# Kernel optimization log

Hardware: AMD Instinct MI355X
Metric: run time of the kernel (lower is better)

The kernel has to match this reference:

```python
import jax, jax.numpy as jnp
import numpy as np

N_NODES = 512   # nodes per graph == feature dim (GCNConv in_channels)
B = 64          # batch of graphs
HID = 16        # action_hidden_dim == edge_hidden_dim
E = 262144      # total edges (~8 per node)
N_TOTAL = B * N_NODES


def _gcn(x, W, b, src, dst, n):
    """PyG GCNConv: add self loops, sym-normalize, x@W -> scatter-add, +bias."""
    h = x @ W  # [n, hid]
    loop = jnp.arange(n)
    s = jnp.concatenate([src, loop])
    d = jnp.concatenate([dst, loop])
    deg = jax.ops.segment_sum(jnp.ones((s.shape[0],), x.dtype), d, num_segments=n)
    dinv = jnp.where(deg > 0, jax.lax.rsqrt(deg), 0.0)
    norm = dinv[s] * dinv[d]
    out = jax.ops.segment_sum(norm[:, None] * h[s], d, num_segments=n)
    return out + b


def _group_sum(t, ptr):
    # cumsum-based segment sum over contiguous node blocks, as in the original
    c = jnp.concatenate([jnp.zeros((1,) + t.shape[1:], t.dtype), jnp.cumsum(t, axis=0)], axis=0)
    return c[ptr[1:]] - c[ptr[:-1]]


def setup_inputs() -> dict:
    key = jax.random.key(0)
    k = jax.random.split(key, 4)
    node_feature = jax.random.normal(k[0], (N_TOTAL, N_NODES), jnp.float32)
    edge_index = jax.random.randint(k[1], (E, 2), 0, N_TOTAL)  # global node ids
    node_index = jnp.arange(N_TOTAL)                            # sorted global ids
    batch_ptr = jnp.arange(B + 1) * N_NODES
    scale = np.float32(1.0 / np.sqrt(N_NODES))
    W_act = jax.random.normal(k[2], (N_NODES, HID), jnp.float32) * scale
    b_act = jnp.zeros((HID,), jnp.float32)
    W_edge = jax.random.normal(k[3], (N_NODES, HID), jnp.float32) * scale
    b_edge = jnp.zeros((HID,), jnp.float32)
    return {"node_feature": node_feature, "W_act": W_act, "b_act": b_act,
            "W_edge": W_edge, "b_edge": b_edge, "edge_index": edge_index,
            "node_index": node_index, "batch_ptr": batch_ptr}


def reference(node_feature, W_act, b_act, W_edge, b_edge, edge_index, node_index, batch_ptr):
    n_total, n_nodes = node_feature.shape
    n_graphs = batch_ptr.shape[0] - 1
    # remap global ids -> local positions; node_index sorted => searchsorted
    # is exactly the original's torch.where(edge_index[...,None]==node_index)[2]
    ei = jnp.searchsorted(node_index, edge_index)  # [E, 2]
    src, dst = ei[:, 0], ei[:, 1]
    # action-type head: GCN -> mean over hidden -> per-graph segment sum
    at = _gcn(node_feature, W_act, b_act, src, dst, n_total)          # [N, hid]
    at = _group_sum(jnp.mean(at, axis=-1, keepdims=True), batch_ptr)  # [B, 1]
    # edge head: GCN -> per-graph pairwise inner products
    eh = _gcn(node_feature, W_edge, b_edge, src, dst, n_total)
    eh = eh.reshape(n_graphs, n_nodes, -1)                            # [B, n, hid]
    pair = jnp.einsum('bnf,bmf->bnm', eh, eh)                         # [B, n, n]
    edge_actions = pair.reshape(n_graphs, n_nodes * n_nodes)
    return jnp.concatenate([at, edge_actions], axis=-1)               # [B, 1 + n*n]
```

## Files before the change

### kernel.cpp

```cpp
#include <hip/hip_runtime.h>
#include <hip/hip_bf16.h>
#include <stdint.h>

#define NTOT   32768
#define NNODE  512
#define NGRAPH 64
#define HID    16
#define NEDGE  262144
#define OROW   262145
#define CAP    32
#define GEMM_BLOCKS 1024

typedef __attribute__((ext_vector_type(4)))  float f32x4;
typedef __attribute__((ext_vector_type(16))) float f32x16;
typedef __attribute__((ext_vector_type(8)))  short bf16x8;

union U8 { bf16x8 v; unsigned int u[4]; };

static __device__ __forceinline__ unsigned int pkbf(float lo, float hi) {
  union { __hip_bfloat162 h; unsigned int u; } c;
  c.h = __float22bfloat162_rn(float2{lo, hi});
  return c.u;
}
static __device__ __forceinline__ unsigned short f2bf(float f) {
  union { float f; unsigned int u; } v; v.f = f;
  unsigned int u = v.u;
  u += 0x7fffu + ((u >> 16) & 1u);
  return (unsigned short)(u >> 16);
}

__global__ __launch_bounds__(512) void k_gemmfill(const float* __restrict__ x,
                                                  const float* __restrict__ Wa,
                                                  const float* __restrict__ We,
                                                  const int* __restrict__ ei,
                                                  int* __restrict__ cnt,
                                                  int* __restrict__ csr,
                                                  float* __restrict__ h_act,
                                                  float* __restrict__ h_edge) {
  __shared__ float red[64 * 129];
  if (blockIdx.x >= GEMM_BLOCKS) {
    int i = (blockIdx.x - GEMM_BLOCKS) * 512 + threadIdx.x;
    int4 e2 = ((const int4*)ei)[i];
    int p0 = atomicAdd(&cnt[e2.y], 1);
    if (p0 < CAP) csr[e2.y * CAP + p0] = e2.x;
    int p1 = atomicAdd(&cnt[e2.w], 1);
    if (p1 < CAP) csr[e2.w * CAP + p1] = e2.z;
    return;
  }
  int row0 = blockIdx.x * 32;
  int w = threadIdx.x >> 6, lane = threadIdx.x & 63;
  int r = lane & 31, g = lane >> 5;
  const float* xp = x + (size_t)(row0 + r) * 512 + w * 64 + g * 8;
  const float* Wp = ((r < 16) ? Wa : We) + (r & 15);
  int k0 = w * 64 + g * 8;
  f32x16 acc = {0,0,0,0,0,0,0,0,0,0,0,0,0,0,0,0};
  #pragma unroll
  for (int kb = 0; kb < 4; ++kb) {
    f32x4 x0 = *(const f32x4*)(xp + kb * 16);
    f32x4 x1 = *(const f32x4*)(xp + kb * 16 + 4);
    U8 a, b;
    a.u[0] = pkbf(x0[0], x0[1]);
    a.u[1] = pkbf(x0[2], x0[3]);
    a.u[2] = pkbf(x1[0], x1[1]);
    a.u[3] = pkbf(x1[2], x1[3]);
    int kk = k0 + kb * 16;
    #pragma unroll
    for (int p = 0; p < 4; ++p)
      b.u[p] = pkbf(Wp[(kk + 2 * p) * 16], Wp[(kk + 2 * p + 1) * 16]);
    acc = __builtin_amdgcn_mfma_f32_32x32x16_bf16(a.v, b.v, acc, 0, 0, 0);
  }
  #pragma unroll
  for (int i = 0; i < 16; ++i) red[lane * 129 + w * 16 + i] = acc[i];
  __syncthreads();
  int rl = threadIdx.x & 63, q = threadIdx.x >> 6;
  float s0 = 0.f, s1 = 0.f;
  #pragma unroll
  for (int ww = 0; ww < 8; ++ww) {
    s0 += red[rl * 129 + ww * 16 + q * 2];
    s1 += red[rl * 129 + ww * 16 + q * 2 + 1];
  }
  int col = rl & 31, gg = rl >> 5;
  float* hp = (col < 16) ? h_act : h_edge;
  int c = col & 15;
  int i0 = q * 2, i1 = i0 + 1;
  hp[(row0 + (i0 & 3) + 8 * (i0 >> 2) + 4 * gg) * HID + c] = s0;
  hp[(row0 + (i1 & 3) + 8 * (i1 >> 2) + 4 * gg) * HID + c] = s1;
}

__global__ __launch_bounds__(256) void k_gather(const int* __restrict__ cnt,
                                                const int* __restrict__ csr,
                                                const float* __restrict__ h_act,
                                                const float* __restrict__ h_edge,
                                                const float* __restrict__ ba,
                                                const float* __restrict__ be,
                                                unsigned short* __restrict__ ebf,
                                                float* __restrict__ at_graph) {
  int tid = blockIdx.x * 256 + threadIdx.x;
  int node = tid >> 4, f = tid & 15;
  int deg = cnt[node];
  float dd = rsqrtf(1.0f + (float)deg);
  int nd = min(deg, CAP);
  float w0 = dd * dd;
  float acc_a = w0 * h_act[(size_t)node * HID + f];
  float acc_e = w0 * h_edge[(size_t)node * HID + f];
  const int* bucket = csr + (size_t)node * CAP;
  for (int k = 0; k < nd; ++k) {
    int s = bucket[k];
    float w = rsqrtf(1.0f + (float)cnt[s]) * dd;
    acc_a += w * h_act[(size_t)s * HID + f];
    acc_e += w * h_edge[(size_t)s * HID + f];
  }
  float va = acc_a + ba[f];
  float ve = acc_e + be[f];
  ebf[tid] = f2bf(ve);
  #pragma unroll
  for (int m = 1; m < 16; m <<= 1) va += __shfl_xor(va, m, 64);
  __shared__ float ablk[16];
  if (f == 0) ablk[threadIdx.x >> 4] = va;
  __syncthreads();
  if (threadIdx.x == 0) {
    float s = 0.f;
    #pragma unroll
    for (int i = 0; i < 16; ++i) s += ablk[i];
    unsafeAtomicAdd(&at_graph[blockIdx.x >> 5], s);
  }
}

__global__ __launch_bounds__(256) void k_gram(const unsigned short* __restrict__ ebf,
                                              const float* __restrict__ at_graph,
                                              float* __restrict__ out) {
  int b = blockIdx.x;
  int graph = b >> 3, sub = b & 7;
  if (sub == 0 && threadIdx.x == 0)
    out[(size_t)graph * OROW] = at_graph[graph] * (1.0f / 16.0f);
  int wave = threadIdx.x >> 6, lane = threadIdx.x & 63;
  int r = lane & 15, g = lane >> 4;
  int n0 = (sub * 4 + wave) * 16;
  const unsigned short* eb = ebf + graph * NNODE * HID;
  size_t obase = (size_t)graph * OROW + 1;
  bf16x8 zf = {0,0,0,0,0,0,0,0};
  bf16x8 a = zf;
  if (g < 2) a = *(const bf16x8*)(eb + (n0 + r) * HID + g * 8);
  for (int mt = 0; mt < 32; ++mt) {
    int m0 = mt * 16;
    bf16x8 bb = zf;
    if (g < 2) bb = *(const bf16x8*)(eb + (m0 + r) * HID + g * 8);
    f32x4 acc = {0, 0, 0, 0};
    acc = __builtin_amdgcn_mfma_f32_16x16x32_bf16(a, bb, acc, 0, 0, 0);
    #pragma unroll
    for (int j = 0; j < 4; ++j) {
      int n = n0 + g * 4 + j;
      out[obase + (size_t)n * NNODE + m0 + r] = acc[j];
    }
  }
}

extern "C" void kernel_launch(void* const* d_in, const int* in_sizes, int n_in,
                              void* d_out, int out_size, void* d_ws, size_t ws_size,
                              hipStream_t stream) {
  const float* x  = (const float*)d_in[0];
  const float* Wa = (const float*)d_in[1];
  const float* ba = (const float*)d_in[2];
  const float* We = (const float*)d_in[3];
  const float* be = (const float*)d_in[4];
  const int* ei   = (const int*)d_in[5];
  float* out = (float*)d_out;

  char* w = (char*)d_ws;
  float* h_act    = (float*)(w);
  float* h_edge   = (float*)(w + (2u << 20));
  unsigned short* ebf = (unsigned short*)(w + (4u << 20));
  int*   csr      = (int*)  (w + (5u << 20));
  int*   cnt      = (int*)  (w + (9u << 20));
  float* at_graph = (float*)(w + (9u << 20) + (128u << 10));

  hipMemsetAsync(cnt, 0, 32768 * 4 + 64 * 4, stream);
  k_gemmfill<<<1280, 512, 0, stream>>>(x, Wa, We, ei, cnt, csr, h_act, h_edge);
  k_gather  <<<2048, 256, 0, stream>>>(cnt, csr, h_act, h_edge, ba, be, ebf, at_graph);
  k_gram    <<<512, 256, 0, stream>>>(ebf, at_graph, out);
}
```

Before: 72.13 us.

## Collapse action head to per-node hidden mean, vectorize CSR loads, split gram blocks

Because the action head only needs the mean over hidden features, the GEMM kernel now reduces the action projection to one scalar per node. The gather kernel then aggregates that scalar instead of a 16-wide vector, and the bias sum is folded into the final per-graph output. The gather loop reads neighbor indices as int4 with masked tails. The gram kernel doubles its grid by splitting columns into halves. The aim is to cut gather memory traffic and raise parallelism in the output-write stage, at the cost of one extra memset and changed float summation order.

```diff
diff --git a/kernel.cpp b/kernel.cpp
--- a/kernel.cpp
+++ b/kernel.cpp
@@ -35,8 +35,8 @@
                                                   const int* __restrict__ ei,
                                                   int* __restrict__ cnt,
                                                   int* __restrict__ csr,
-                                                  float* __restrict__ h_act,
-                                                  float* __restrict__ h_edge) {
+                                                  float* __restrict__ h_edge,
+                                                  float* __restrict__ hm) {
   __shared__ float red[64 * 129];
   if (blockIdx.x >= GEMM_BLOCKS) {
     int i = (blockIdx.x - GEMM_BLOCKS) * 512 + threadIdx.x;
@@ -79,19 +79,30 @@
     s0 += red[rl * 129 + ww * 16 + q * 2];
     s1 += red[rl * 129 + ww * 16 + q * 2 + 1];
   }
+  float t0 = s0, t1 = s1;
+  #pragma unroll
+  for (int m = 1; m < 16; m <<= 1) {
+    t0 += __shfl_xor(t0, m, 64);
+    t1 += __shfl_xor(t1, m, 64);
+  }
   int col = rl & 31, gg = rl >> 5;
-  float* hp = (col < 16) ? h_act : h_edge;
-  int c = col & 15;
   int i0 = q * 2, i1 = i0 + 1;
-  hp[(row0 + (i0 & 3) + 8 * (i0 >> 2) + 4 * gg) * HID + c] = s0;
-  hp[(row0 + (i1 & 3) + 8 * (i1 >> 2) + 4 * gg) * HID + c] = s1;
+  int ro0 = (i0 & 3) + 8 * (i0 >> 2) + 4 * gg;
+  int ro1 = (i1 & 3) + 8 * (i1 >> 2) + 4 * gg;
+  if (col >= 16) {
+    h_edge[(row0 + ro0) * HID + (col - 16)] = s0;
+    h_edge[(row0 + ro1) * HID + (col - 16)] = s1;
+  }
+  if ((rl & 31) == 0) {
+    hm[row0 + ro0] = t0;
+    hm[row0 + ro1] = t1;
+  }
 }
 
 __global__ __launch_bounds__(256) void k_gather(const int* __restrict__ cnt,
                                                 const int* __restrict__ csr,
-                                                const float* __restrict__ h_act,
                                                 const float* __restrict__ h_edge,
-                                                const float* __restrict__ ba,
+                                                const float* __restrict__ hm,
                                                 const float* __restrict__ be,
                                                 unsigned short* __restrict__ ebf,
                                                 float* __restrict__ at_graph) {
@@ -101,20 +112,23 @@
   float dd = rsqrtf(1.0f + (float)deg);
   int nd = min(deg, CAP);
   float w0 = dd * dd;
-  float acc_a = w0 * h_act[(size_t)node * HID + f];
   float acc_e = w0 * h_edge[(size_t)node * HID + f];
-  const int* bucket = csr + (size_t)node * CAP;
-  for (int k = 0; k < nd; ++k) {
-    int s = bucket[k];
-    float w = rsqrtf(1.0f + (float)cnt[s]) * dd;
-    acc_a += w * h_act[(size_t)s * HID + f];
-    acc_e += w * h_edge[(size_t)s * HID + f];
-  }
-  float va = acc_a + ba[f];
-  float ve = acc_e + be[f];
-  ebf[tid] = f2bf(ve);
-  #pragma unroll
-  for (int m = 1; m < 16; m <<= 1) va += __shfl_xor(va, m, 64);
+  float va    = w0 * hm[node];
+  const int4* b4 = (const int4*)(csr + (size_t)node * CAP);
+  for (int k4 = 0; k4 * 4 < nd; ++k4) {
+    int4 s4 = b4[k4];
+    int ss[4] = {s4.x, s4.y, s4.z, s4.w};
+    #pragma unroll
+    for (int j = 0; j < 4; ++j) {
+      int kk = k4 * 4 + j;
+      bool on = kk < nd;
+      int s = on ? ss[j] : node;
+      float w = on ? rsqrtf(1.0f + (float)cnt[s]) * dd : 0.0f;
+      acc_e += w * h_edge[(size_t)s * HID + f];
+      va    += w * hm[s];
+    }
+  }
+  ebf[tid] = f2bf(acc_e + be[f]);
   __shared__ float ablk[16];
   if (f == 0) ablk[threadIdx.x >> 4] = va;
   __syncthreads();
@@ -128,11 +142,16 @@
 
 __global__ __launch_bounds__(256) void k_gram(const unsigned short* __restrict__ ebf,
                                               const float* __restrict__ at_graph,
+                                              const float* __restrict__ ba,
                                               float* __restrict__ out) {
   int b = blockIdx.x;
-  int graph = b >> 3, sub = b & 7;
-  if (sub == 0 && threadIdx.x == 0)
-    out[(size_t)graph * OROW] = at_graph[graph] * (1.0f / 16.0f);
+  int graph = b >> 4, sub = (b >> 1) & 7, half = b & 1;
+  if (sub == 0 && half == 0 && threadIdx.x == 0) {
+    float sb = 0.f;
+    #pragma unroll
+    for (int f = 0; f < 16; ++f) sb += ba[f];
+    out[(size_t)graph * OROW] = (at_graph[graph] + 512.0f * sb) * (1.0f / 16.0f);
+  }
   int wave = threadIdx.x >> 6, lane = threadIdx.x & 63;
   int r = lane & 15, g = lane >> 4;
   int n0 = (sub * 4 + wave) * 16;
@@ -141,7 +160,7 @@
   bf16x8 zf = {0,0,0,0,0,0,0,0};
   bf16x8 a = zf;
   if (g < 2) a = *(const bf16x8*)(eb + (n0 + r) * HID + g * 8);
-  for (int mt = 0; mt < 32; ++mt) {
+  for (int mt = half * 16; mt < half * 16 + 16; ++mt) {
     int m0 = mt * 16;
     bf16x8 bb = zf;
     if (g < 2) bb = *(const bf16x8*)(eb + (m0 + r) * HID + g * 8);
@@ -167,15 +186,16 @@
   float* out = (float*)d_out;
 
   char* w = (char*)d_ws;
-  float* h_act    = (float*)(w);
-  float* h_edge   = (float*)(w + (2u << 20));
-  unsigned short* ebf = (unsigned short*)(w + (4u << 20));
-  int*   csr      = (int*)  (w + (5u << 20));
-  int*   cnt      = (int*)  (w + (9u << 20));
-  float* at_graph = (float*)(w + (9u << 20) + (128u << 10));
-
-  hipMemsetAsync(cnt, 0, 32768 * 4 + 64 * 4, stream);
-  k_gemmfill<<<1280, 512, 0, stream>>>(x, Wa, We, ei, cnt, csr, h_act, h_edge);
-  k_gather  <<<2048, 256, 0, stream>>>(cnt, csr, h_act, h_edge, ba, be, ebf, at_graph);
-  k_gram    <<<512, 256, 0, stream>>>(ebf, at_graph, out);
-}
+  float* h_edge   = (float*)(w);
+  unsigned short* ebf = (unsigned short*)(w + (2u << 20));
+  int*   csr      = (int*)  (w + (3u << 20));
+  int*   cnt      = (int*)  (w + (7u << 20));
+  float* hm       = (float*)(w + (7u << 20) + (128u << 10));
+  float* at_graph = (float*)(w + (7u << 20) + (256u << 10));
+
+  hipMemsetAsync(cnt, 0, 32768 * 4, stream);
+  hipMemsetAsync(at_graph, 0, 64 * 4, stream);
+  k_gemmfill<<<1280, 512, 0, stream>>>(x, Wa, We, ei, cnt, csr, h_edge, hm);
+  k_gather  <<<2048, 256, 0, stream>>>(cnt, csr, h_edge, hm, be, ebf, at_graph);
+  k_gram    <<<1024, 256, 0, stream>>>(ebf, at_graph, ba, out);
+}
```

Result: no change. 71.04 us (-1.5%).
